# Performance work log

Hardware: AMD Instinct MI355X
Metric: run time of the kernel (lower is better)

## Reference

```python
import jax, jax.numpy as jnp
import numpy as np

DM = 768            # d_model
DI = 1536           # d_inner = expand * d_model
P = 64              # headdim
H = DI // P         # 24 heads
N = 64              # d_state (Mamba2Simple default)
K = 4               # d_conv
CONVD = DI + 2 * N  # 1664
D_IN_PROJ = 2 * DI + 2 * N + H  # 3224
BATCH = 2
NVAL = 1024
L = NVAL
EPS = 1e-5

# static tail_order / swap_order index (transpose the rows x cols token grid, reversed)
_rows = int(NVAL ** 0.5)
_t = np.arange(NVAL).reshape(_rows, -1).T
_t = NVAL - 1 - _t
TAIL = _t.reshape(-1)
SEQ = jnp.asarray(np.concatenate([np.arange(L - NVAL), TAIL + (L - NVAL)]))


def _make_params(key, prefix):
    ks = jax.random.split(key, 6)
    dt = jnp.exp(jax.random.uniform(ks[2], (H,), minval=np.log(1e-3), maxval=np.log(1e-1)))
    return {
        prefix + 'ln_w': jnp.ones(DM, jnp.float32),
        prefix + 'ln_b': jnp.zeros(DM, jnp.float32),
        prefix + 'in_w': jax.random.normal(ks[0], (D_IN_PROJ, DM), jnp.float32) * 0.02,
        prefix + 'conv_w': jax.random.normal(ks[1], (CONVD, K), jnp.float32) * 0.1,
        prefix + 'conv_b': jnp.zeros(CONVD, jnp.float32),
        prefix + 'dt_bias': jnp.log(jnp.expm1(dt)),  # inverse softplus of dt in [1e-3, 1e-1]
        prefix + 'A_log': jnp.log(jax.random.uniform(ks[3], (H,), minval=1.0, maxval=16.0)),
        prefix + 'D': jnp.ones(H, jnp.float32),
        prefix + 'norm_w': jnp.ones(DI, jnp.float32),
        prefix + 'out_w': jax.random.normal(ks[4], (DM, DI), jnp.float32) * 0.02,
    }


def setup_inputs() -> dict:
    key = jax.random.key(0)
    k1, k2, k3 = jax.random.split(key, 3)
    inp = {'x': jax.random.normal(k1, (BATCH, L, DM), dtype=jnp.float32)}
    inp.update(_make_params(k2, 'f_'))
    inp.update(_make_params(k3, 'b_'))
    return inp


def _layernorm(x, w, b):
    m = jnp.mean(x, -1, keepdims=True)
    v = jnp.mean((x - m) ** 2, -1, keepdims=True)
    return (x - m) * jax.lax.rsqrt(v + EPS) * w + b


def _mamba2(x, in_w, conv_w, conv_b, dt_bias, A_log, Dp, norm_w, out_w):
    Bsz, Lseq, _ = x.shape
    zxbcdt = x @ in_w.T                                   # [B,L,3224]
    z, xBC, dt = jnp.split(zxbcdt, [DI, DI + CONVD], axis=-1)
    dt = jax.nn.softplus(dt + dt_bias)                    # [B,L,H]
    # causal depthwise conv1d over channels
    xc = jnp.transpose(xBC, (0, 2, 1))                    # [B,C,L]
    xc = jax.lax.conv_general_dilated(xc, conv_w[:, None, :], (1,), [(K - 1, 0)],
                                      feature_group_count=CONVD)
    xBC = jax.nn.silu(jnp.transpose(xc, (0, 2, 1)) + conv_b)
    xs, Bm, Cm = jnp.split(xBC, [DI, DI + N], axis=-1)
    xs = xs.reshape(Bsz, Lseq, H, P)
    A = -jnp.exp(A_log)                                   # [H], negative

    def step(S, inp):
        dt_t, x_t, B_t, C_t = inp                         # [B,H],[B,H,P],[B,N],[B,N]
        dA = jnp.exp(dt_t * A)                            # [B,H]
        S = S * dA[..., None, None] + dt_t[..., None, None] * B_t[:, None, :, None] * x_t[:, :, None, :]
        y = jnp.einsum('bn,bhnp->bhp', C_t, S)
        return S, y

    S0 = jnp.zeros((Bsz, H, N, P), x.dtype)
    ins = (jnp.moveaxis(dt, 1, 0), jnp.moveaxis(xs, 1, 0),
           jnp.moveaxis(Bm, 1, 0), jnp.moveaxis(Cm, 1, 0))
    _, ys = jax.lax.scan(step, S0, ins)
    y = jnp.moveaxis(ys, 0, 1) + Dp[None, None, :, None] * xs  # D skip, [B,L,H,P]
    y = y.reshape(Bsz, Lseq, DI)
    # RMSNormGated: gate then rmsnorm
    y = y * jax.nn.silu(z)
    y = y * jax.lax.rsqrt(jnp.mean(y * y, -1, keepdims=True) + EPS) * norm_w
    return y @ out_w.T


def _wrap(x, ln_w, ln_b, *mp):
    return x + _mamba2(_layernorm(x, ln_w, ln_b), *mp)


def reference(x,
              f_ln_w, f_ln_b, f_in_w, f_conv_w, f_conv_b, f_dt_bias, f_A_log, f_D, f_norm_w, f_out_w,
              b_ln_w, b_ln_b, b_in_w, b_conv_w, b_conv_b, b_dt_bias, b_A_log, b_D, b_norm_w, b_out_w):
    left_right = _wrap(x, f_ln_w, f_ln_b, f_in_w, f_conv_w, f_conv_b, f_dt_bias, f_A_log, f_D, f_norm_w, f_out_w)
    xs = x[:, SEQ]
    down_up = _wrap(xs, b_ln_w, b_ln_b, b_in_w, b_conv_w, b_conv_b, b_dt_bias, b_A_log, b_D, b_norm_w, b_out_w)
    down_up = down_up[:, SEQ]
    return left_right + down_up
```

## Files before the change

### kernel.cpp

```cpp
#include <hip/hip_runtime.h>
#include <cstdint>

#define DM    768
#define DI    1536
#define PP    64
#define HH    24
#define NN    64
#define NP1   3328
#define LL    1024
#define ROWS  2048
#define DINP  3224
#define EPSF  1e-5f
#define NCHUNK 16
#define CLEN   64

typedef unsigned short ushortT;
typedef __attribute__((ext_vector_type(8))) __bf16 bf16x8;
typedef __attribute__((ext_vector_type(8))) unsigned short ushort8;
typedef __attribute__((ext_vector_type(4))) unsigned short ushort4v;
typedef __attribute__((ext_vector_type(4))) float f32x4;

__device__ __forceinline__ int seqmap(int t) { return 1023 - 32 * (t & 31) - (t >> 5); }

__device__ __forceinline__ ushortT f2bf(float f) {
  union { float f; unsigned u; } v; v.f = f;
  unsigned r = v.u + 0x7FFF + ((v.u >> 16) & 1);
  return (ushortT)(r >> 16);
}
__device__ __forceinline__ float bf2f(ushortT b) {
  union { unsigned u; float f; } v; v.u = ((unsigned)b) << 16;
  return v.f;
}

__device__ __forceinline__ void gload_lds16(const void* g, void* l) {
  __builtin_amdgcn_global_load_lds((const __attribute__((address_space(1))) void*)g,
                                   (__attribute__((address_space(3))) void*)l, 16, 0, 0);
}

#define SWZ(r, c) ((r) * 64 + ((c) ^ (((r) & 7) << 3)))
#define SWZ64(r, c) ((r) * 64 + ((c) ^ (((r) & 7) << 3)))

__global__ __launch_bounds__(256) void prep_kernel(const float* __restrict__ x,
    const float* __restrict__ wf, const float* __restrict__ bf_,
    const float* __restrict__ wb, const float* __restrict__ bb,
    ushortT* __restrict__ xln, float* __restrict__ out,
    const float* __restrict__ fw1, const float* __restrict__ bw1,
    const float* __restrict__ fw2, const float* __restrict__ bw2,
    ushortT* __restrict__ WP1, ushortT* __restrict__ W2) {
  __shared__ float lds[4];
  int bid = blockIdx.x;
  int tid = threadIdx.x;
  if (bid < 2048) {
    int b = bid >> 10, sr = bid & 1023;
    const float* xr = x + (size_t)bid * DM;
    float v0 = xr[tid], v1 = xr[tid + 256], v2 = xr[tid + 512];
    float* outp = out + (size_t)bid * DM;
    outp[tid] = 2.f * v0; outp[tid + 256] = 2.f * v1; outp[tid + 512] = 2.f * v2;
    float s = v0 + v1 + v2;
    #pragma unroll
    for (int o = 32; o; o >>= 1) s += __shfl_xor(s, o, 64);
    if ((tid & 63) == 0) lds[tid >> 6] = s;
    __syncthreads();
    float mean = (lds[0] + lds[1] + lds[2] + lds[3]) * (1.f / 768.f);
    __syncthreads();
    float d0 = v0 - mean, d1 = v1 - mean, d2 = v2 - mean;
    float q = d0 * d0 + d1 * d1 + d2 * d2;
    #pragma unroll
    for (int o = 32; o; o >>= 1) q += __shfl_xor(q, o, 64);
    if ((tid & 63) == 0) lds[tid >> 6] = q;
    __syncthreads();
    float var = (lds[0] + lds[1] + lds[2] + lds[3]) * (1.f / 768.f);
    float rs = rsqrtf(var + EPSF);
    int t1 = seqmap(sr);
    ushortT* o0 = xln + (size_t)bid * DM;
    ushortT* o1 = xln + (size_t)(2048 + b * 1024 + t1) * DM;
    o0[tid]       = f2bf(d0 * rs * wf[tid]       + bf_[tid]);
    o0[tid + 256] = f2bf(d1 * rs * wf[tid + 256] + bf_[tid + 256]);
    o0[tid + 512] = f2bf(d2 * rs * wf[tid + 512] + bf_[tid + 512]);
    o1[tid]       = f2bf(d0 * rs * wb[tid]       + bb[tid]);
    o1[tid + 256] = f2bf(d1 * rs * wb[tid + 256] + bb[tid + 256]);
    o1[tid + 512] = f2bf(d2 * rs * wb[tid + 512] + bb[tid + 512]);
  } else {
    const long NW1 = (long)NP1 * DM, SW1 = (long)DINP * DM, NW2 = (long)DM * DI;
    const long tot8 = (2 * NW1 + 2 * NW2) >> 3;
    long nb = (long)gridDim.x - 2048;
    for (long i8 = (long)(bid - 2048) * 256 + tid; i8 < tot8; i8 += nb * 256) {
      long i = i8 << 3;
      const float* src = nullptr;
      ushortT* dst;
      if (i < NW1) {
        if (i < SW1) src = fw1 + i;
        dst = WP1 + i;
      } else if (i < 2 * NW1) {
        long j = i - NW1;
        if (j < SW1) src = bw1 + j;
        dst = WP1 + i;
      } else if (i < 2 * NW1 + NW2) {
        long j = i - 2 * NW1;
        src = fw2 + j;
        dst = W2 + j;
      } else {
        long j = i - 2 * NW1 - NW2;
        src = bw2 + j;
        dst = W2 + NW2 + j;
      }
      ushort8 o = {};
      if (src) {
        float4 a = *(const float4*)src;
        float4 b2 = *(const float4*)(src + 4);
        o[0] = f2bf(a.x);  o[1] = f2bf(a.y);  o[2] = f2bf(a.z);  o[3] = f2bf(a.w);
        o[4] = f2bf(b2.x); o[5] = f2bf(b2.y); o[6] = f2bf(b2.z); o[7] = f2bf(b2.w);
      }
      *(ushort8*)dst = o;
    }
  }
}

template<int MODE>
__global__ __launch_bounds__(256) void gemm_bf16(
    const ushortT* __restrict__ Aall, const ushortT* __restrict__ Ball,
    float* __restrict__ Cfall, ushortT* __restrict__ Cball,
    int K, int lda, int ldb, int ldc, long sA, long sB, long sCf, long sCb) {
  __shared__ ushortT sA2[2][128 * 64];
  __shared__ ushortT sB2[2][128 * 64];
  int gx = gridDim.x, gy = gridDim.y;
  int nwg = gx * gy * gridDim.z;
  int lid = blockIdx.x + gx * (blockIdx.y + gy * blockIdx.z);
  int cpx = nwg >> 3;
  int swz = (lid & 7) * cpx + (lid >> 3);
  int bx = swz % gx;
  int rest = swz / gx;
  int by = rest % gy, bz = rest / gy;
  const ushortT* A = Aall + (size_t)bz * sA;
  const ushortT* B = Ball + (size_t)bz * sB;
  int tid = threadIdx.x, lane = tid & 63, w = tid >> 6;
  int wm = w >> 1, wn = w & 1;
  int m0 = by * 128, n0 = bx * 128;
  int rA8 = lane >> 3;
  int cSw = ((lane & 7) << 3) ^ (((lane >> 3) & 7) << 3);
  f32x4 acc[4][4] = {};
  const int NT = K >> 6;
  int fr = lane & 15, kq = lane >> 4;

  auto STAGE = [&](int bf, int kt) {
    int kc = kt * 64 + cSw;
    #pragma unroll
    for (int c2 = 0; c2 < 4; ++c2) {
      int q = w * 4 + c2;
      gload_lds16(A + (size_t)(m0 + q * 8 + rA8) * lda + kc, &sA2[bf][q * 512]);
    }
    #pragma unroll
    for (int c2 = 0; c2 < 4; ++c2) {
      int q = w * 4 + c2;
      gload_lds16(B + (size_t)(n0 + q * 8 + rA8) * ldb + kc, &sB2[bf][q * 512]);
    }
  };

  STAGE(0, 0);
  int cur = 0;
  for (int kt = 0; kt < NT; ++kt) {
    if (kt + 1 < NT) {
      STAGE(cur ^ 1, kt + 1);
      asm volatile("s_waitcnt vmcnt(8)" ::: "memory");
    } else {
      asm volatile("s_waitcnt vmcnt(0)" ::: "memory");
    }
    __builtin_amdgcn_s_barrier();
    __builtin_amdgcn_sched_barrier(0);
    #pragma unroll
    for (int ks = 0; ks < 2; ++ks) {
      int kb = ks * 32 + kq * 8;
      bf16x8 af[4], bfr[4];
      #pragma unroll
      for (int i = 0; i < 4; ++i)
        af[i] = *(const bf16x8*)&sA2[cur][SWZ64(wm * 64 + i * 16 + fr, kb)];
      #pragma unroll
      for (int j = 0; j < 4; ++j)
        bfr[j] = *(const bf16x8*)&sB2[cur][SWZ64(wn * 64 + j * 16 + fr, kb)];
      #pragma unroll
      for (int i = 0; i < 4; ++i)
        #pragma unroll
        for (int j = 0; j < 4; ++j)
          acc[i][j] = __builtin_amdgcn_mfma_f32_16x16x32_bf16(af[i], bfr[j], acc[i][j], 0, 0, 0);
    }
    asm volatile("s_waitcnt lgkmcnt(0)" ::: "memory");
    __builtin_amdgcn_sched_barrier(0);
    __builtin_amdgcn_s_barrier();
    cur ^= 1;
  }
  int cr = (lane >> 4) * 4, cc = lane & 15;
  if (MODE == 1 && n0 >= 3200) {
    float* Cf = Cfall + (size_t)bz * sCf;
    #pragma unroll
    for (int i = 0; i < 4; ++i)
      #pragma unroll
      for (int j = 0; j < 4; ++j) {
        float* Cp = Cf + (size_t)(m0 + wm * 64 + i * 16 + cr) * 128 + (wn * 64 + j * 16 + cc);
        #pragma unroll
        for (int r = 0; r < 4; ++r) Cp[(size_t)r * 128] = acc[i][j][r];
      }
  } else if (MODE == 2) {
    #pragma unroll
    for (int i = 0; i < 4; ++i)
      #pragma unroll
      for (int r = 0; r < 4; ++r) {
        int mrow = m0 + wm * 64 + i * 16 + cr + r;
        int brow;
        if (bz == 0) brow = mrow;
        else { int bb2 = mrow >> 10, tt2 = mrow & 1023; brow = bb2 * 1024 + seqmap(tt2); }
        float* orow = Cfall + (size_t)brow * DM;
        #pragma unroll
        for (int j = 0; j < 4; ++j)
          atomicAdd(&orow[n0 + wn * 64 + j * 16 + cc], acc[i][j][r]);
      }
  } else {
    ushortT* Cb = Cball + (size_t)bz * sCb;
    #pragma unroll
    for (int i = 0; i < 4; ++i)
      #pragma unroll
      for (int j = 0; j < 4; ++j) {
        ushortT* Cp = Cb + (size_t)(m0 + wm * 64 + i * 16 + cr) * ldc + (n0 + wn * 64 + j * 16 + cc);
        #pragma unroll
        for (int r = 0; r < 4; ++r) Cp[(size_t)r * ldc] = f2bf(acc[i][j][r]);
      }
  }
}

__global__ __launch_bounds__(256) void convbc_kernel(const ushortT* __restrict__ zxb,
    const float* __restrict__ cwf, const float* __restrict__ cbf,
    const float* __restrict__ cwb, const float* __restrict__ cbb,
    ushortT* __restrict__ bcc) {
  __shared__ ushortT sZ[67 * 128];
  int chunk = blockIdx.x, dirb = blockIdx.y;
  int dir = dirb >> 1;
  int t0 = chunk * 64;
  size_t rowb = (size_t)dirb * 1024;
  const float* cw = dir ? cwb : cwf;
  const float* cb = dir ? cbb : cbf;
  int tid = threadIdx.x;
  for (int idx = tid; idx < 67 * 16; idx += 256) {
    int r = idx >> 4, g = idx & 15;
    int t = t0 - 3 + r;
    ushort8 v = {};
    if (t >= 0) v = *(const ushort8*)&zxb[(rowb + t) * NP1 + 3072 + g * 8];
    *(ushort8*)&sZ[r * 128 + g * 8] = v;
  }
  __syncthreads();
  ushortT* outB = bcc + ((size_t)(dirb * NCHUNK + chunk) * 2) * 4096;
  ushortT* outC = outB + 4096;
  for (int idx = tid; idx < 64 * 16; idx += 256) {
    int r = idx >> 4, g = idx & 15;
    int cc8 = g * 8;
    ushort8 x0 = *(const ushort8*)&sZ[(r + 0) * 128 + cc8];
    ushort8 x1 = *(const ushort8*)&sZ[(r + 1) * 128 + cc8];
    ushort8 x2 = *(const ushort8*)&sZ[(r + 2) * 128 + cc8];
    ushort8 x3 = *(const ushort8*)&sZ[(r + 3) * 128 + cc8];
    ushort8 o;
    #pragma unroll
    for (int e = 0; e < 8; ++e) {
      int gc = 1536 + cc8 + e;
      float a = cb[gc] + bf2f(x0[e]) * cw[gc * 4 + 0] + bf2f(x1[e]) * cw[gc * 4 + 1]
              + bf2f(x2[e]) * cw[gc * 4 + 2] + bf2f(x3[e]) * cw[gc * 4 + 3];
      o[e] = f2bf(a / (1.f + __expf(-a)));
    }
    if (cc8 < 64) *(ushort8*)&outB[SWZ(r, cc8)] = o;
    else          *(ushort8*)&outC[SWZ(r, cc8 - 64)] = o;
  }
}

__global__ __launch_bounds__(256) void ssd_chunk_kernel(const ushortT* __restrict__ zxb,
    const ushortT* __restrict__ bcc,
    const float* __restrict__ dtt,
    const float* __restrict__ cwf, const float* __restrict__ cbf,
    const float* __restrict__ cwb, const float* __restrict__ cbb,
    const float* __restrict__ dtbf, const float* __restrict__ alogf,
    const float* __restrict__ dtbb, const float* __restrict__ alogb,
    const float* __restrict__ Df, const float* __restrict__ Db,
    ushortT* __restrict__ yb, ushortT* __restrict__ slocb, float* __restrict__ cwg) {
  __shared__ ushortT sCb[4096];
  __shared__ ushortT sBb[4096];
  __shared__ ushortT sXT[4096];
  __shared__ ushortT sPool[8192];
  __shared__ float clog[64];
  __shared__ float dt64[64];
  __shared__ float wv64[64];
  ushortT* sBT   = sPool;
  ushortT* sMb   = sPool + 4096;
  ushortT* sRawX = sPool;

  int gh = blockIdx.x;
  int c  = blockIdx.y;
  int dir = gh / 48;
  int rem = gh % 48;
  int b = rem / 24, h = rem % 24;
  int tid = threadIdx.x, lane = tid & 63;
  int w = tid >> 6;
  int dirb = dir * 2 + b;
  size_t rowbase = (size_t)dirb * 1024;
  int t0 = c * CLEN;
  size_t trow = rowbase + (size_t)t0;
  const float* cw   = dir ? cwb : cwf;
  const float* cb   = dir ? cbb : cbf;
  const float* dtb  = dir ? dtbb : dtbf;
  const float* alog = dir ? alogb : alogf;
  float Dv = (dir ? Db : Df)[h];

  {
    const ushortT* bSrc = bcc + ((size_t)(dirb * NCHUNK + c) * 2) * 4096;
    const ushortT* cSrc = bSrc + 4096;
    #pragma unroll
    for (int ph = 0; ph < 2; ++ph) {
      int base = ph * 2048 + w * 512;
      gload_lds16(bSrc + base + lane * 8, &sBb[base]);
      gload_lds16(cSrc + base + lane * 8, &sCb[base]);
    }
  }
  for (int idx = tid; idx < 67 * 8; idx += 256) {
    int r = idx >> 3, g = idx & 7;
    int t = t0 - 3 + r;
    ushort8 v = {};
    if (t >= 0) v = *(const ushort8*)&zxb[(rowbase + t) * NP1 + 1536 + h * 64 + g * 8];
    *(ushort8*)&sRawX[r * 72 + g * 8] = v;
  }
  if (tid < 64) {
    float raw = dtt[(trow + tid) * 128 + h] + dtb[h];
    float dtv = raw > 20.f ? raw : log1pf(expf(raw));
    float ld = -expf(alog[h]) * dtv;
    float v = ld;
    #pragma unroll
    for (int o = 1; o < 64; o <<= 1) {
      float u = __shfl_up(v, o, 64);
      if (tid >= o) v += u;
    }
    float tot = __shfl(v, 63, 64);
    clog[tid] = v;
    dt64[tid] = dtv;
    wv64[tid] = dtv * __expf(tot - v);
    cwg[(trow + tid) * HH + h] = __expf(v);
  }
  __syncthreads();

  {
    int p = lane;
    int ch = h * 64 + p;
    float cbv = cb[ch];
    float w0 = cw[ch * 4], w1 = cw[ch * 4 + 1], w2 = cw[ch * 4 + 2], w3 = cw[ch * 4 + 3];
    #pragma unroll
    for (int q = 0; q < 4; ++q) {
      int t4 = w * 16 + q * 4;
      float rv[7];
      #pragma unroll
      for (int rr = 0; rr < 7; ++rr) rv[rr] = bf2f(sRawX[(t4 + rr) * 72 + p]);
      ushort4v v4;
      #pragma unroll
      for (int i = 0; i < 4; ++i) {
        float a = cbv + rv[i] * w0 + rv[i + 1] * w1 + rv[i + 2] * w2 + rv[i + 3] * w3;
        v4[i] = f2bf(a / (1.f + __expf(-a)));
      }
      int cT = t4 ^ ((p & 7) << 3);
      *(ushort4v*)&sXT[p * 64 + cT] = v4;
    }
  }
  __syncthreads();

  int fr = lane & 15, kq = lane >> 4;

  {
    int n = lane;
    #pragma unroll
    for (int q = 0; q < 4; ++q) {
      int s4 = w * 16 + q * 4;
      float b0 = bf2f(sBb[SWZ(s4 + 0, n)]) * wv64[s4 + 0];
      float b1 = bf2f(sBb[SWZ(s4 + 1, n)]) * wv64[s4 + 1];
      float b2 = bf2f(sBb[SWZ(s4 + 2, n)]) * wv64[s4 + 2];
      float b3 = bf2f(sBb[SWZ(s4 + 3, n)]) * wv64[s4 + 3];
      int cT = s4 ^ ((n & 7) << 3);
      ushort4v v4 = {f2bf(b0), f2bf(b1), f2bf(b2), f2bf(b3)};
      *(ushort4v*)&sBT[n * 64 + cT] = v4;
    }
  }
  f32x4 accG[4] = {};
  #pragma unroll
  for (int kt = 0; kt < 2; ++kt) {
    int kk = kt * 32 + kq * 8;
    bf16x8 af = *(const bf16x8*)&sCb[SWZ(w * 16 + fr, kk)];
    #pragma unroll
    for (int j = 0; j < 4; ++j) {
      bf16x8 bf_ = *(const bf16x8*)&sBb[SWZ(j * 16 + fr, kk)];
      accG[j] = __builtin_amdgcn_mfma_f32_16x16x32_bf16(af, bf_, accG[j], 0, 0, 0);
    }
  }
  #pragma unroll
  for (int j = 0; j < 4; ++j) {
    int s = j * 16 + fr;
    float cls = clog[s], dtv = dt64[s];
    #pragma unroll
    for (int r = 0; r < 4; ++r) {
      int t = w * 16 + kq * 4 + r;
      float dec = (s <= t) ? __expf(clog[t] - cls) * dtv : 0.f;
      sMb[SWZ(t, s)] = f2bf(accG[j][r] * dec);
    }
  }
  __syncthreads();

  f32x4 accY[4] = {}, accS[4] = {};
  #pragma unroll
  for (int kt = 0; kt < 2; ++kt) {
    int kk = kt * 32 + kq * 8;
    bf16x8 aM = *(const bf16x8*)&sMb[SWZ(w * 16 + fr, kk)];
    bf16x8 aB = *(const bf16x8*)&sBT[SWZ(w * 16 + fr, kk)];
    #pragma unroll
    for (int j = 0; j < 4; ++j) {
      bf16x8 bx = *(const bf16x8*)&sXT[SWZ(j * 16 + fr, kk)];
      accY[j] = __builtin_amdgcn_mfma_f32_16x16x32_bf16(aM, bx, accY[j], 0, 0, 0);
      accS[j] = __builtin_amdgcn_mfma_f32_16x16x32_bf16(aB, bx, accS[j], 0, 0, 0);
    }
  }
  ushortT* spb = slocb + ((size_t)gh * NCHUNK + c) * 4096;
  #pragma unroll
  for (int j = 0; j < 4; ++j) {
    #pragma unroll
    for (int r = 0; r < 4; ++r) {
      int t = w * 16 + kq * 4 + r;
      int p = j * 16 + fr;
      float xval = bf2f(sXT[SWZ(p, t)]);
      yb[(trow + t) * DI + h * 64 + p] = f2bf(accY[j][r] + Dv * xval);
      spb[t * 64 + p] = f2bf(accS[j][r]);
    }
  }
}

__global__ __launch_bounds__(256) void chunk_prefix_kernel(
    const ushortT* __restrict__ slocb, const float* __restrict__ cwg,
    ushortT* __restrict__ sinitb) {
  __shared__ float ldsT[64 * 65];
  int gh = blockIdx.x;
  int dir = gh / 48;
  int rem = gh % 48;
  int b = rem / 24, h = rem % 24;
  int tid = threadIdx.x;
  size_t rowbase = ((size_t)dir * 2 + b) * 1024;
  float R[16];
  #pragma unroll
  for (int j = 0; j < 16; ++j) R[j] = 0.f;
  for (int c = 1; c < NCHUNK; ++c) {
    float W = cwg[(rowbase + (size_t)c * CLEN - 1) * HH + h];
    const ushortT* slot = slocb + ((size_t)gh * NCHUNK + (c - 1)) * 4096;
    #pragma unroll
    for (int j = 0; j < 16; ++j) {
      int idx = j * 256 + tid, n = idx >> 6, p = idx & 63;
      R[j] = __builtin_fmaf(R[j], W, bf2f(slot[idx]));
      ldsT[n * 65 + p] = R[j];
    }
    __syncthreads();
    ushortT* outp = sinitb + ((size_t)gh * (NCHUNK - 1) + (c - 1)) * 4096;
    #pragma unroll
    for (int j = 0; j < 16; ++j) {
      int idx = j * 256 + tid, p = idx >> 6, n = idx & 63;
      outp[SWZ(p, n)] = f2bf(ldsT[n * 65 + p]);
    }
    __syncthreads();
  }
}

__global__ __launch_bounds__(256) void fixup_kernel(
    const ushortT* __restrict__ bcc, const ushortT* __restrict__ sinitb,
    const float* __restrict__ cwg, ushortT* __restrict__ yb) {
  __shared__ ushortT sCb[4096];
  __shared__ ushortT sST[4096];
  int gh = blockIdx.x;
  int c = blockIdx.y + 1;
  int dir = gh / 48;
  int rem = gh % 48;
  int b = rem / 24, h = rem % 24;
  int tid = threadIdx.x, lane = tid & 63, w = tid >> 6;
  int dirb = dir * 2 + b;
  size_t rowbase = (size_t)dirb * 1024;
  size_t trow = rowbase + (size_t)c * CLEN;
  const ushortT* cbSrc = bcc + ((size_t)(dirb * NCHUNK + c) * 2 + 1) * 4096;
  const ushortT* stSrc = sinitb + ((size_t)gh * (NCHUNK - 1) + (c - 1)) * 4096;
  #pragma unroll
  for (int ph = 0; ph < 2; ++ph) {
    int base = ph * 2048 + w * 512;
    gload_lds16(cbSrc + base + lane * 8, &sCb[base]);
    gload_lds16(stSrc + base + lane * 8, &sST[base]);
  }
  __syncthreads();
  int fr = lane & 15, kq = lane >> 4;
  f32x4 accY[4] = {};
  #pragma unroll
  for (int kt = 0; kt < 2; ++kt) {
    int kk = kt * 32 + kq * 8;
    bf16x8 aC = *(const bf16x8*)&sCb[SWZ(w * 16 + fr, kk)];
    #pragma unroll
    for (int j = 0; j < 4; ++j) {
      bf16x8 bS = *(const bf16x8*)&sST[SWZ(j * 16 + fr, kk)];
      accY[j] = __builtin_amdgcn_mfma_f32_16x16x32_bf16(aC, bS, accY[j], 0, 0, 0);
    }
  }
  float cwv[4];
  #pragma unroll
  for (int r = 0; r < 4; ++r)
    cwv[r] = cwg[(trow + w * 16 + kq * 4 + r) * HH + h];
  #pragma unroll
  for (int j = 0; j < 4; ++j)
    #pragma unroll
    for (int r = 0; r < 4; ++r) {
      int t = w * 16 + kq * 4 + r, p = j * 16 + fr;
      size_t yi = (trow + t) * DI + h * 64 + p;
      yb[yi] = f2bf(bf2f(yb[yi]) + accY[j][r] * cwv[r]);
    }
}

__global__ __launch_bounds__(192) void gate_norm_kernel(
    const ushortT* __restrict__ yb,
    const ushortT* __restrict__ zxb,
    const float* __restrict__ nwf, const float* __restrict__ nwb,
    ushortT* __restrict__ yn) {
  __shared__ float lds[3];
  int bid = blockIdx.x;
  int dir = bid >> 11;
  const float* nw = dir ? nwb : nwf;
  int tid = threadIdx.x;
  int c0 = tid * 8;
  float v[8];
  float ss = 0.f;
  {
    ushort8 yv8 = *(const ushort8*)&yb[(size_t)bid * DI + c0];
    ushort8 zv8 = *(const ushort8*)&zxb[(size_t)bid * NP1 + c0];
    #pragma unroll
    for (int e = 0; e < 8; ++e) {
      float yv = bf2f(yv8[e]);
      float zv = bf2f(zv8[e]);
      yv *= zv / (1.f + expf(-zv));
      v[e] = yv;
      ss += yv * yv;
    }
  }
  #pragma unroll
  for (int o = 32; o; o >>= 1) ss += __shfl_xor(ss, o, 64);
  if ((tid & 63) == 0) lds[tid >> 6] = ss;
  __syncthreads();
  float ms = (lds[0] + lds[1] + lds[2]) * (1.f / 1536.f);
  float sc = rsqrtf(ms + EPSF);
  {
    ushort8 o8;
    #pragma unroll
    for (int e = 0; e < 8; ++e) o8[e] = f2bf(v[e] * sc * nw[c0 + e]);
    *(ushort8*)&yn[(size_t)bid * DI + c0] = o8;
  }
}

extern "C" void kernel_launch(void* const* d_in, const int* in_sizes, int n_in,
                              void* d_out, int out_size, void* d_ws, size_t ws_size,
                              hipStream_t stream) {
  const float* x       = (const float*)d_in[0];
  const float* f_ln_w  = (const float*)d_in[1];
  const float* f_ln_b  = (const float*)d_in[2];
  const float* f_in_w  = (const float*)d_in[3];
  const float* f_cw    = (const float*)d_in[4];
  const float* f_cb    = (const float*)d_in[5];
  const float* f_dtb   = (const float*)d_in[6];
  const float* f_alog  = (const float*)d_in[7];
  const float* f_D     = (const float*)d_in[8];
  const float* f_nw    = (const float*)d_in[9];
  const float* f_ow    = (const float*)d_in[10];
  const float* b_ln_w  = (const float*)d_in[11];
  const float* b_ln_b  = (const float*)d_in[12];
  const float* b_in_w  = (const float*)d_in[13];
  const float* b_cw    = (const float*)d_in[14];
  const float* b_cb    = (const float*)d_in[15];
  const float* b_dtb   = (const float*)d_in[16];
  const float* b_alog  = (const float*)d_in[17];
  const float* b_D     = (const float*)d_in[18];
  const float* b_nw    = (const float*)d_in[19];
  const float* b_ow    = (const float*)d_in[20];
  float* out = (float*)d_out;

  char* ws = (char*)d_ws;
  size_t off = 0;
  auto carve = [&](size_t bytes) -> char* {
    off = (off + 255) & ~(size_t)255;
    char* p = ws + off;
    off += bytes;
    return p;
  };
  ushortT* XLN   = (ushortT*)carve((size_t)2 * ROWS * DM * 2);
  ushortT* WP1   = (ushortT*)carve((size_t)2 * NP1 * DM * 2);
  ushortT* W2    = (ushortT*)carve((size_t)2 * DM * DI * 2);
  ushortT* ZXB   = (ushortT*)carve((size_t)2 * ROWS * NP1 * 2);
  float*   DTT   = (float*)carve((size_t)2 * ROWS * 128 * 4);
  ushortT* YB    = (ushortT*)carve((size_t)2 * ROWS * DI * 2);
  ushortT* YN    = (ushortT*)carve((size_t)2 * ROWS * DI * 2);
  ushortT* SLOCB = (ushortT*)carve((size_t)96 * NCHUNK * 4096 * 2);
  ushortT* SINIB = (ushortT*)carve((size_t)96 * (NCHUNK - 1) * 4096 * 2);
  ushortT* BCC   = (ushortT*)carve((size_t)4 * NCHUNK * 2 * 4096 * 2);
  float*   CWG   = (float*)carve((size_t)2 * ROWS * HH * 4);

  prep_kernel<<<4096, 256, 0, stream>>>(x, f_ln_w, f_ln_b, b_ln_w, b_ln_b, XLN, out,
                                        f_in_w, b_in_w, f_ow, b_ow, WP1, W2);

  gemm_bf16<1><<<dim3(NP1 / 128, ROWS / 128, 2), 256, 0, stream>>>(
      XLN, WP1, DTT, ZXB, DM, DM, DM, NP1,
      (long)ROWS * DM, (long)NP1 * DM, (long)ROWS * 128, (long)ROWS * NP1);

  convbc_kernel<<<dim3(NCHUNK, 4), 256, 0, stream>>>(ZXB, f_cw, f_cb, b_cw, b_cb, BCC);

  ssd_chunk_kernel<<<dim3(96, NCHUNK), 256, 0, stream>>>(
      ZXB, BCC, DTT, f_cw, f_cb, b_cw, b_cb, f_dtb, f_alog, b_dtb, b_alog,
      f_D, b_D, YB, SLOCB, CWG);

  chunk_prefix_kernel<<<96, 256, 0, stream>>>(SLOCB, CWG, SINIB);
  fixup_kernel<<<dim3(96, NCHUNK - 1), 256, 0, stream>>>(BCC, SINIB, CWG, YB);

  gate_norm_kernel<<<4096, 192, 0, stream>>>(YB, ZXB, f_nw, b_nw, YN);

  gemm_bf16<2><<<dim3(DM / 128, ROWS / 128, 2), 256, 0, stream>>>(
      YN, W2, out, nullptr, DI, DI, DI, DM,
      (long)ROWS * DI, (long)DM * DI, 0, 0);
}
```

Measured before the change: 145.8 us.

## Fuse chunk prefix with fixup and replace atomic output GEMM with combine pass

Merges the chunk-prefix and fixup kernels into a single per-head kernel that builds each chunk's initial state in LDS and applies the inter-chunk correction right away, so the state buffer no longer makes a round trip through global memory. It also drops the fp32 atomicAdd epilogue of the output GEMM. The GEMM now writes bf16 results, and a separate combine kernel adds 2x plus the forward and permuted backward outputs. The cost is less parallelism in the inter-chunk step (96 blocks run 15 chunks serially), an extra launch, and bf16 rounding of the GEMM outputs.

```diff
diff --git a/kernel.cpp b/kernel.cpp
--- a/kernel.cpp
+++ b/kernel.cpp
@@ -43,7 +43,7 @@
 __global__ __launch_bounds__(256) void prep_kernel(const float* __restrict__ x,
     const float* __restrict__ wf, const float* __restrict__ bf_,
     const float* __restrict__ wb, const float* __restrict__ bb,
-    ushortT* __restrict__ xln, float* __restrict__ out,
+    ushortT* __restrict__ xln,
     const float* __restrict__ fw1, const float* __restrict__ bw1,
     const float* __restrict__ fw2, const float* __restrict__ bw2,
     ushortT* __restrict__ WP1, ushortT* __restrict__ W2) {
@@ -54,8 +54,6 @@
     int b = bid >> 10, sr = bid & 1023;
     const float* xr = x + (size_t)bid * DM;
     float v0 = xr[tid], v1 = xr[tid + 256], v2 = xr[tid + 512];
-    float* outp = out + (size_t)bid * DM;
-    outp[tid] = 2.f * v0; outp[tid + 256] = 2.f * v1; outp[tid + 512] = 2.f * v2;
     float s = v0 + v1 + v2;
     #pragma unroll
     for (int o = 32; o; o >>= 1) s += __shfl_xor(s, o, 64);
@@ -199,20 +197,6 @@
         #pragma unroll
         for (int r = 0; r < 4; ++r) Cp[(size_t)r * 128] = acc[i][j][r];
       }
-  } else if (MODE == 2) {
-    #pragma unroll
-    for (int i = 0; i < 4; ++i)
-      #pragma unroll
-      for (int r = 0; r < 4; ++r) {
-        int mrow = m0 + wm * 64 + i * 16 + cr + r;
-        int brow;
-        if (bz == 0) brow = mrow;
-        else { int bb2 = mrow >> 10, tt2 = mrow & 1023; brow = bb2 * 1024 + seqmap(tt2); }
-        float* orow = Cfall + (size_t)brow * DM;
-        #pragma unroll
-        for (int j = 0; j < 4; ++j)
-          atomicAdd(&orow[n0 + wn * 64 + j * 16 + cc], acc[i][j][r]);
-      }
   } else {
     ushortT* Cb = Cball + (size_t)bz * sCb;
     #pragma unroll
@@ -430,86 +414,73 @@
   }
 }
 
-__global__ __launch_bounds__(256) void chunk_prefix_kernel(
-    const ushortT* __restrict__ slocb, const float* __restrict__ cwg,
-    ushortT* __restrict__ sinitb) {
+__global__ __launch_bounds__(256) void inter_kernel(
+    const ushortT* __restrict__ slocb, const ushortT* __restrict__ bcc,
+    const float* __restrict__ cwg, ushortT* __restrict__ yb) {
   __shared__ float ldsT[64 * 65];
+  __shared__ ushortT sST[4096];
+  __shared__ ushortT sCb[4096];
   int gh = blockIdx.x;
-  int dir = gh / 48;
-  int rem = gh % 48;
-  int b = rem / 24, h = rem % 24;
-  int tid = threadIdx.x;
-  size_t rowbase = ((size_t)dir * 2 + b) * 1024;
-  float R[16];
-  #pragma unroll
-  for (int j = 0; j < 16; ++j) R[j] = 0.f;
-  for (int c = 1; c < NCHUNK; ++c) {
-    float W = cwg[(rowbase + (size_t)c * CLEN - 1) * HH + h];
-    const ushortT* slot = slocb + ((size_t)gh * NCHUNK + (c - 1)) * 4096;
-    #pragma unroll
-    for (int j = 0; j < 16; ++j) {
-      int idx = j * 256 + tid, n = idx >> 6, p = idx & 63;
-      R[j] = __builtin_fmaf(R[j], W, bf2f(slot[idx]));
-      ldsT[n * 65 + p] = R[j];
-    }
-    __syncthreads();
-    ushortT* outp = sinitb + ((size_t)gh * (NCHUNK - 1) + (c - 1)) * 4096;
-    #pragma unroll
-    for (int j = 0; j < 16; ++j) {
-      int idx = j * 256 + tid, p = idx >> 6, n = idx & 63;
-      outp[SWZ(p, n)] = f2bf(ldsT[n * 65 + p]);
-    }
-    __syncthreads();
-  }
-}
-
-__global__ __launch_bounds__(256) void fixup_kernel(
-    const ushortT* __restrict__ bcc, const ushortT* __restrict__ sinitb,
-    const float* __restrict__ cwg, ushortT* __restrict__ yb) {
-  __shared__ ushortT sCb[4096];
-  __shared__ ushortT sST[4096];
-  int gh = blockIdx.x;
-  int c = blockIdx.y + 1;
   int dir = gh / 48;
   int rem = gh % 48;
   int b = rem / 24, h = rem % 24;
   int tid = threadIdx.x, lane = tid & 63, w = tid >> 6;
   int dirb = dir * 2 + b;
   size_t rowbase = (size_t)dirb * 1024;
-  size_t trow = rowbase + (size_t)c * CLEN;
-  const ushortT* cbSrc = bcc + ((size_t)(dirb * NCHUNK + c) * 2 + 1) * 4096;
-  const ushortT* stSrc = sinitb + ((size_t)gh * (NCHUNK - 1) + (c - 1)) * 4096;
+  int fr = lane & 15, kq = lane >> 4;
+  float R[16];
   #pragma unroll
-  for (int ph = 0; ph < 2; ++ph) {
-    int base = ph * 2048 + w * 512;
-    gload_lds16(cbSrc + base + lane * 8, &sCb[base]);
-    gload_lds16(stSrc + base + lane * 8, &sST[base]);
-  }
-  __syncthreads();
-  int fr = lane & 15, kq = lane >> 4;
-  f32x4 accY[4] = {};
-  #pragma unroll
-  for (int kt = 0; kt < 2; ++kt) {
-    int kk = kt * 32 + kq * 8;
-    bf16x8 aC = *(const bf16x8*)&sCb[SWZ(w * 16 + fr, kk)];
-    #pragma unroll
-    for (int j = 0; j < 4; ++j) {
-      bf16x8 bS = *(const bf16x8*)&sST[SWZ(j * 16 + fr, kk)];
-      accY[j] = __builtin_amdgcn_mfma_f32_16x16x32_bf16(aC, bS, accY[j], 0, 0, 0);
-    }
-  }
-  float cwv[4];
-  #pragma unroll
-  for (int r = 0; r < 4; ++r)
-    cwv[r] = cwg[(trow + w * 16 + kq * 4 + r) * HH + h];
-  #pragma unroll
-  for (int j = 0; j < 4; ++j)
-    #pragma unroll
-    for (int r = 0; r < 4; ++r) {
-      int t = w * 16 + kq * 4 + r, p = j * 16 + fr;
-      size_t yi = (trow + t) * DI + h * 64 + p;
-      yb[yi] = f2bf(bf2f(yb[yi]) + accY[j][r] * cwv[r]);
-    }
+  for (int j = 0; j < 16; ++j) R[j] = 0.f;
+  for (int c = 1; c < NCHUNK; ++c) {
+    {
+      const ushortT* cbSrc = bcc + ((size_t)(dirb * NCHUNK + c) * 2 + 1) * 4096;
+      #pragma unroll
+      for (int ph = 0; ph < 2; ++ph) {
+        int base = ph * 2048 + w * 512;
+        gload_lds16(cbSrc + base + lane * 8, &sCb[base]);
+      }
+    }
+    float W = cwg[(rowbase + (size_t)c * CLEN - 1) * HH + h];
+    const ushortT* slot = slocb + ((size_t)gh * NCHUNK + (c - 1)) * 4096;
+    #pragma unroll
+    for (int j = 0; j < 16; ++j) {
+      int idx = j * 256 + tid, n = idx >> 6, p = idx & 63;
+      R[j] = __builtin_fmaf(R[j], W, bf2f(slot[idx]));
+      ldsT[n * 65 + p] = R[j];
+    }
+    __syncthreads();
+    #pragma unroll
+    for (int j = 0; j < 16; ++j) {
+      int idx = j * 256 + tid, p2 = idx >> 6, n2 = idx & 63;
+      sST[SWZ(p2, n2)] = f2bf(ldsT[n2 * 65 + p2]);
+    }
+    __syncthreads();
+    size_t trow = rowbase + (size_t)c * CLEN;
+    f32x4 accY[4] = {};
+    #pragma unroll
+    for (int kt = 0; kt < 2; ++kt) {
+      int kk = kt * 32 + kq * 8;
+      bf16x8 aC = *(const bf16x8*)&sCb[SWZ(w * 16 + fr, kk)];
+      #pragma unroll
+      for (int j = 0; j < 4; ++j) {
+        bf16x8 bS = *(const bf16x8*)&sST[SWZ(j * 16 + fr, kk)];
+        accY[j] = __builtin_amdgcn_mfma_f32_16x16x32_bf16(aC, bS, accY[j], 0, 0, 0);
+      }
+    }
+    float cwv[4];
+    #pragma unroll
+    for (int r = 0; r < 4; ++r)
+      cwv[r] = cwg[(trow + w * 16 + kq * 4 + r) * HH + h];
+    #pragma unroll
+    for (int j = 0; j < 4; ++j)
+      #pragma unroll
+      for (int r = 0; r < 4; ++r) {
+        int t = w * 16 + kq * 4 + r, p = j * 16 + fr;
+        size_t yi = (trow + t) * DI + h * 64 + p;
+        yb[yi] = f2bf(bf2f(yb[yi]) + accY[j][r] * cwv[r]);
+      }
+    __syncthreads();
+  }
 }
 
 __global__ __launch_bounds__(192) void gate_norm_kernel(
@@ -549,6 +520,32 @@
     for (int e = 0; e < 8; ++e) o8[e] = f2bf(v[e] * sc * nw[c0 + e]);
     *(ushort8*)&yn[(size_t)bid * DI + c0] = o8;
   }
+}
+
+__global__ __launch_bounds__(128) void combine_kernel(const float* __restrict__ x,
+    const ushortT* __restrict__ mf, const ushortT* __restrict__ mb,
+    float* __restrict__ out) {
+  int bid = blockIdx.x;
+  int b = bid >> 10, t = bid & 1023;
+  int st = seqmap(t);
+  int tid = threadIdx.x;
+  if (tid >= 96) return;
+  int c0 = tid * 8;
+  ushort8 fv = *(const ushort8*)&mf[(size_t)bid * DM + c0];
+  ushort8 bv = *(const ushort8*)&mb[(size_t)(b * 1024 + st) * DM + c0];
+  const float4 x0 = *(const float4*)&x[(size_t)bid * DM + c0];
+  const float4 x1 = *(const float4*)&x[(size_t)bid * DM + c0 + 4];
+  float4 o0, o1;
+  o0.x = 2.f * x0.x + bf2f(fv[0]) + bf2f(bv[0]);
+  o0.y = 2.f * x0.y + bf2f(fv[1]) + bf2f(bv[1]);
+  o0.z = 2.f * x0.z + bf2f(fv[2]) + bf2f(bv[2]);
+  o0.w = 2.f * x0.w + bf2f(fv[3]) + bf2f(bv[3]);
+  o1.x = 2.f * x1.x + bf2f(fv[4]) + bf2f(bv[4]);
+  o1.y = 2.f * x1.y + bf2f(fv[5]) + bf2f(bv[5]);
+  o1.z = 2.f * x1.z + bf2f(fv[6]) + bf2f(bv[6]);
+  o1.w = 2.f * x1.w + bf2f(fv[7]) + bf2f(bv[7]);
+  *(float4*)&out[(size_t)bid * DM + c0] = o0;
+  *(float4*)&out[(size_t)bid * DM + c0 + 4] = o1;
 }
 
 extern "C" void kernel_launch(void* const* d_in, const int* in_sizes, int n_in,
@@ -592,12 +589,12 @@
   float*   DTT   = (float*)carve((size_t)2 * ROWS * 128 * 4);
   ushortT* YB    = (ushortT*)carve((size_t)2 * ROWS * DI * 2);
   ushortT* YN    = (ushortT*)carve((size_t)2 * ROWS * DI * 2);
+  ushortT* MOUTB = (ushortT*)carve((size_t)2 * ROWS * DM * 2);
   ushortT* SLOCB = (ushortT*)carve((size_t)96 * NCHUNK * 4096 * 2);
-  ushortT* SINIB = (ushortT*)carve((size_t)96 * (NCHUNK - 1) * 4096 * 2);
   ushortT* BCC   = (ushortT*)carve((size_t)4 * NCHUNK * 2 * 4096 * 2);
   float*   CWG   = (float*)carve((size_t)2 * ROWS * HH * 4);
 
-  prep_kernel<<<4096, 256, 0, stream>>>(x, f_ln_w, f_ln_b, b_ln_w, b_ln_b, XLN, out,
+  prep_kernel<<<4096, 256, 0, stream>>>(x, f_ln_w, f_ln_b, b_ln_w, b_ln_b, XLN,
                                         f_in_w, b_in_w, f_ow, b_ow, WP1, W2);
 
   gemm_bf16<1><<<dim3(NP1 / 128, ROWS / 128, 2), 256, 0, stream>>>(
@@ -610,12 +607,13 @@
       ZXB, BCC, DTT, f_cw, f_cb, b_cw, b_cb, f_dtb, f_alog, b_dtb, b_alog,
       f_D, b_D, YB, SLOCB, CWG);
 
-  chunk_prefix_kernel<<<96, 256, 0, stream>>>(SLOCB, CWG, SINIB);
-  fixup_kernel<<<dim3(96, NCHUNK - 1), 256, 0, stream>>>(BCC, SINIB, CWG, YB);
+  inter_kernel<<<96, 256, 0, stream>>>(SLOCB, BCC, CWG, YB);
 
   gate_norm_kernel<<<4096, 192, 0, stream>>>(YB, ZXB, f_nw, b_nw, YN);
 
-  gemm_bf16<2><<<dim3(DM / 128, ROWS / 128, 2), 256, 0, stream>>>(
-      YN, W2, out, nullptr, DI, DI, DI, DM,
-      (long)ROWS * DI, (long)DM * DI, 0, 0);
-}
+  gemm_bf16<0><<<dim3(DM / 128, ROWS / 128, 2), 256, 0, stream>>>(
+      YN, W2, nullptr, MOUTB, DI, DI, DI, DM,
+      (long)ROWS * DI, (long)DM * DI, 0, (long)ROWS * DM);
+
+  combine_kernel<<<2048, 128, 0, stream>>>(x, MOUTB, MOUTB + (size_t)ROWS * DM, out);
+}
```

New measurement: 201.3 us. 1.38x slower.
